# Kernel tuning notes

Measured on AMD Instinct MI355X. Metric: run time of the kernel, lower is better.

The kernel has to match this reference:

```python
import jax, jax.numpy as jnp
import numpy as np
import math

D_MODEL = 2048
NUM_HEADS = 16
D_HEAD = D_MODEL // NUM_HEADS
ROPE_BASE = 10000.0

def _rope(t, pos):
    # t: [b, h, T, d_head]; standard rotate-half RoPE with base 10000.
    T, d = t.shape[-2], t.shape[-1]
    start = max(pos, 0)  # pos < 0 means training / position 0
    inv_freq = 1.0 / (ROPE_BASE ** (jnp.arange(0, d, 2, dtype=jnp.float32) / d))  # [d/2]
    positions = jnp.arange(start, start + T, dtype=jnp.float32)                   # [T]
    ang = positions[:, None] * inv_freq[None, :]                                  # [T, d/2]
    cos, sin = jnp.cos(ang), jnp.sin(ang)
    x1, x2 = t[..., : d // 2], t[..., d // 2 :]
    return jnp.concatenate([x1 * cos - x2 * sin, x1 * sin + x2 * cos], axis=-1)

def setup_inputs() -> dict:
    key = jax.random.key(0)
    kx, kq, kk, kv, kw = jax.random.split(key, 5)
    s = 1.0 / math.sqrt(D_MODEL)
    return {
        "x": jax.random.normal(kx, (2, 2048, D_MODEL), dtype=jnp.float32),
        "q_out": jax.random.normal(kq, (D_MODEL, D_MODEL), dtype=jnp.float32) * s,
        "k_out": jax.random.normal(kk, (D_MODEL, D_MODEL), dtype=jnp.float32) * s,
        "v_out": jax.random.normal(kv, (D_MODEL, D_MODEL), dtype=jnp.float32) * s,
        "w_out": jax.random.normal(kw, (D_MODEL, D_MODEL), dtype=jnp.float32) * s,
        "pos": 0,
    }

def reference(x, q_out, k_out, v_out, w_out, pos):
    b, t, d = x.shape
    h, dh = NUM_HEADS, D_HEAD

    def heads(y):  # [b, t, d] -> [b, h, t, dh]
        return y.reshape(b, t, h, dh).transpose(0, 2, 1, 3)

    q = _rope(heads(jnp.einsum('btd,de->bte', x, q_out)), pos)
    k = _rope(heads(jnp.einsum('btd,de->bte', x, k_out)), pos)
    v = heads(jnp.einsum('btd,de->bte', x, v_out))

    score = jnp.einsum('bhqd,bhkd->bhqk', q, k) / math.sqrt(dh)
    causal = jnp.triu(jnp.ones((t, t), dtype=bool), k=1)  # True above diagonal -> masked
    score = jnp.where(causal, -jnp.inf, score)
    weights = jax.nn.softmax(score, axis=-1)
    ctx = jnp.einsum('bhqk,bhkd->bhqd', weights, v)        # [b, h, t, dh]
    ctx = ctx.transpose(0, 2, 1, 3).reshape(b, t, d)
    return jnp.einsum('btd,de->bte', ctx, w_out)
```

## Files before the change

kernel.cpp:

```cpp
#include <hip/hip_runtime.h>
#include <hip/hip_bf16.h>
#include <math.h>

#define NH 16
#define DH 128
#define DM 2048
#define BB 2
#define TT 2048

typedef unsigned short u16;
typedef __attribute__((ext_vector_type(8))) __bf16 bf16x8;
typedef __attribute__((ext_vector_type(8))) u16 u16x8;
typedef __attribute__((ext_vector_type(4))) u16 u16x4;
typedef __attribute__((ext_vector_type(4))) float f32x4;

__device__ __forceinline__ float bf2f(u16 a){
  union { unsigned u; float f; } v; v.u = ((unsigned)a) << 16; return v.f;
}
__device__ __forceinline__ u16 f2bf(float f){
  union { float f; unsigned u; } v; v.f = f;
  unsigned r = v.u + 0x7fffu + ((v.u >> 16) & 1u);
  return (u16)(r >> 16);
}
__device__ __forceinline__ __bf16 f2bfh(float f){
  u16 r = f2bf(f); __bf16 h; __builtin_memcpy(&h, &r, 2); return h;
}
__device__ __forceinline__ float bfh2f(__bf16 h){
  u16 r; __builtin_memcpy(&r, &h, 2); return bf2f(r);
}

typedef const __attribute__((address_space(1))) unsigned int* gas_p;
typedef __attribute__((address_space(3))) unsigned int* las_p;
__device__ __forceinline__ void gl_lds16(const u16* g, u16* lds_uniform_base){
  __builtin_amdgcn_global_load_lds((gas_p)(const void*)g,
                                   (las_p)(void*)lds_uniform_base, 16, 0, 0);
}

#define SB() do{ asm volatile("" ::: "memory"); \
                 __builtin_amdgcn_s_barrier();  \
                 asm volatile("" ::: "memory"); }while(0)
#define WAITV8 asm volatile("s_waitcnt vmcnt(8)" ::: "memory")
#define WAITV0 asm volatile("s_waitcnt vmcnt(0)" ::: "memory")

__global__ __launch_bounds__(256)
void prep4(const float* __restrict__ w0, const float* __restrict__ w1,
           const float* __restrict__ w2, const float* __restrict__ x,
           u16* __restrict__ dst, u16* __restrict__ xb){
  __shared__ u16 tile[32][33];
  const int z = blockIdx.z;
  const int tx = threadIdx.x, ty = threadIdx.y;
  if (z == 3){
    const int bid = blockIdx.y * 64 + blockIdx.x;
    const int tid = ty * 32 + tx;
    #pragma unroll
    for (int rep = 0; rep < 2; rep++){
      const int i = bid * 512 + rep * 256 + tid;
      const f32x4 v = *(const f32x4*)(x + (size_t)i * 4);
      u16x4 o;
      #pragma unroll
      for (int j = 0; j < 4; j++) o[j] = f2bf(v[j]);
      *(u16x4*)(xb + (size_t)i * 4) = o;
    }
    return;
  }
  const float* W = (z == 0) ? w0 : (z == 1) ? w1 : w2;
  u16* Wt = dst + (size_t)z * DM * DM;
  const int bx = blockIdx.x * 32, by = blockIdx.y * 32;
  #pragma unroll
  for (int i = 0; i < 32; i += 8)
    tile[ty + i][tx] = f2bf(W[(size_t)(by + ty + i) * DM + bx + tx]);
  __syncthreads();
  #pragma unroll
  for (int i = 0; i < 32; i += 8)
    Wt[(size_t)(bx + ty + i) * DM + by + tx] = tile[tx][ty + i];
}

__global__ __launch_bounds__(256)
void transpose2048(const float* __restrict__ W, u16* __restrict__ Wt){
  __shared__ u16 tile[32][33];
  const int tx = threadIdx.x, ty = threadIdx.y;
  const int bx = blockIdx.x * 32, by = blockIdx.y * 32;
  #pragma unroll
  for (int i = 0; i < 32; i += 8)
    tile[ty + i][tx] = f2bf(W[(size_t)(by + ty + i) * DM + bx + tx]);
  __syncthreads();
  #pragma unroll
  for (int i = 0; i < 32; i += 8)
    Wt[(size_t)(bx + ty + i) * DM + by + tx] = tile[tx][ty + i];
}

__global__ __launch_bounds__(256)
void cvt_f32_bf16(const float* __restrict__ src, u16* __restrict__ dst, int n4){
  const int i = blockIdx.x * 256 + threadIdx.x;
  if (i >= n4) return;
  const f32x4 v = *(const f32x4*)(src + (size_t)i * 4);
  u16x4 o;
  #pragma unroll
  for (int j = 0; j < 4; j++) o[j] = f2bf(v[j]);
  *(u16x4*)(dst + (size_t)i * 4) = o;
}

__global__ __launch_bounds__(256)
void gemm_bt(const u16* __restrict__ A, const u16* __restrict__ Bt_base,
             void* __restrict__ C0, u16* __restrict__ Ck, u16* __restrict__ Cv,
             int mode0){
  __shared__ u16 As[2][128][32];
  __shared__ u16 Bs[2][128][32];
  const int z = blockIdx.z;
  const u16* Bt = Bt_base + (size_t)z * DM * DM;
  void* C = (z == 0) ? C0 : (z == 1) ? (void*)Ck : (void*)Cv;
  const int mode = (z == 0) ? mode0 : (z == 1) ? 3 : 2;

  const int tid = threadIdx.x;
  const int wave = tid >> 6, lane = tid & 63;
  const int wm = wave & 1, wn = wave >> 1;
  const int row16 = lane & 15, quad = lane >> 4;
  const int m0 = blockIdx.x * 128, n0 = blockIdx.y * 128;

  const f32x4 zero = {0.f, 0.f, 0.f, 0.f};
  f32x4 acc[4][4];
  #pragma unroll
  for (int i = 0; i < 4; i++)
    #pragma unroll
    for (int j = 0; j < 4; j++) acc[i][j] = zero;

  const int srow = lane >> 2;
  const int scol = (lane & 3) * 8;

  for (int k0 = 0; k0 < DM; k0 += 64){
    #pragma unroll
    for (int c = 0; c < 2; c++){
      const int rbase = wave * 32 + c * 16;
      const u16* pa = A  + (size_t)(m0 + rbase + srow) * DM + k0 + scol;
      const u16* pb = Bt + (size_t)(n0 + rbase + srow) * DM + k0 + scol;
      gl_lds16(pa,      &As[0][rbase][0]);
      gl_lds16(pa + 32, &As[1][rbase][0]);
      gl_lds16(pb,      &Bs[0][rbase][0]);
      gl_lds16(pb + 32, &Bs[1][rbase][0]);
    }
    __syncthreads();
    #pragma unroll
    for (int buf = 0; buf < 2; buf++){
      bf16x8 af[4], bfr[4];
      #pragma unroll
      for (int mt = 0; mt < 4; mt++)
        af[mt] = *(const bf16x8*)&As[buf][wm * 64 + mt * 16 + row16][quad * 8];
      #pragma unroll
      for (int nt = 0; nt < 4; nt++)
        bfr[nt] = *(const bf16x8*)&Bs[buf][wn * 64 + nt * 16 + row16][quad * 8];
      #pragma unroll
      for (int mt = 0; mt < 4; mt++)
        #pragma unroll
        for (int nt = 0; nt < 4; nt++)
          acc[mt][nt] = __builtin_amdgcn_mfma_f32_16x16x32_bf16(af[mt], bfr[nt], acc[mt][nt], 0, 0, 0);
    }
    __syncthreads();
  }

  #pragma unroll
  for (int mt = 0; mt < 4; mt++){
    #pragma unroll
    for (int nt = 0; nt < 4; nt++){
      #pragma unroll
      for (int r = 0; r < 4; r++){
        const int m = m0 + wm * 64 + mt * 16 + quad * 4 + r;
        const int n = n0 + wn * 64 + nt * 16 + row16;
        const int b = m >> 11, t = m & (TT - 1);
        const int hh = n >> 7, dh = n & (DH - 1);
        if (mode == 1){
          ((u16*)C)[(((size_t)(b * NH + hh) * TT + t) * DH) + dh] = f2bf(acc[mt][nt][r]);
        } else if (mode == 3){
          const int dhs = dh ^ ((t & 7) << 3);
          ((u16*)C)[(((size_t)(b * NH + hh) * TT + t) * DH) + dhs] = f2bf(acc[mt][nt][r]);
        } else if (mode == 2){
          const int ts = (t & 63) ^ ((dh & 7) << 3);
          ((u16*)C)[(((size_t)(b * NH + hh) * 32 + (t >> 6)) * 8192) + dh * 64 + ts] = f2bf(acc[mt][nt][r]);
        } else {
          ((float*)C)[(size_t)m * DM + n] = acc[mt][nt][r];
        }
      }
    }
  }
}

__global__ __launch_bounds__(256)
void ropek(u16* __restrict__ kb, const int* __restrict__ posp){
  const int idx = blockIdx.x * 256 + threadIdx.x;
  const int pair = idx & 63;
  const int row = idx >> 6;
  const int t = row & (TT - 1);
  int p0 = *posp; if (p0 < 0) p0 = 0;
  const float tf = (float)(p0 + t);
  const size_t base = (size_t)row * DH;
  const int pl = pair ^ ((t & 7) << 3);
  const float inv = __expf(-(float)pl * (9.2103403719761836f / 64.f));
  const float a = tf * inv;
  const float sn = __sinf(a), cs = __cosf(a);
  const float k1 = bf2f(kb[base + pair]);
  const float k2 = bf2f(kb[base + 64 + pair]);
  kb[base + pair]      = f2bf(k1 * cs - k2 * sn);
  kb[base + 64 + pair] = f2bf(k1 * sn + k2 * cs);
}

template<bool MASK>
__device__ __forceinline__ void attn_tile(
    int kt0, int qbase, int wave, int row16, int quad,
    const bf16x8 (&qf)[4],
    u16 (&k_s)[64][128], u16 (&vt_s)[128][64], u16 (&p_s)[4][16][68],
    f32x4 (&o_acc)[8], float (&l_acc)[4])
{
  const float scale = 0.08838834764831845f;
  const f32x4 zero = {0.f, 0.f, 0.f, 0.f};
  const int fx = (row16 & 7) << 3;
  f32x4 s_acc[4];
  #pragma unroll
  for (int nt = 0; nt < 4; nt++) s_acc[nt] = zero;
  __builtin_amdgcn_s_setprio(1);
  #pragma unroll
  for (int st = 0; st < 4; st++)
    #pragma unroll
    for (int nt = 0; nt < 4; nt++){
      const bf16x8 kf = *(const bf16x8*)&k_s[nt * 16 + row16][(st * 32 + quad * 8) ^ fx];
      s_acc[nt] = __builtin_amdgcn_mfma_f32_16x16x32_bf16(qf[st], kf, s_acc[nt], 0, 0, 0);
    }
  __builtin_amdgcn_s_setprio(0);
  #pragma unroll
  for (int r = 0; r < 4; r++){
    float ps = 0.f;
    #pragma unroll
    for (int nt = 0; nt < 4; nt++){
      float p = __expf(s_acc[nt][r] * scale);
      if (MASK){
        const int qr = qbase + quad * 4 + r;
        if (kt0 + nt * 16 + row16 > qr) p = 0.f;
      }
      ps += p;
      p_s[wave][quad * 4 + r][nt * 16 + row16] = f2bf(p);
    }
    l_acc[r] += ps;
  }
  asm volatile("" ::: "memory");

  __builtin_amdgcn_s_setprio(1);
  #pragma unroll
  for (int kk = 0; kk < 2; kk++){
    const bf16x8 pf = *(const bf16x8*)&p_s[wave][row16][kk * 32 + quad * 8];
    #pragma unroll
    for (int nd = 0; nd < 8; nd++){
      const bf16x8 vb = *(const bf16x8*)&vt_s[nd * 16 + row16][(kk * 32 + quad * 8) ^ fx];
      o_acc[nd] = __builtin_amdgcn_mfma_f32_16x16x32_bf16(pf, vb, o_acc[nd], 0, 0, 0);
    }
  }
  __builtin_amdgcn_s_setprio(0);
}

__device__ __forceinline__ void attn_pass(
    const u16* __restrict__ q, const u16* __restrict__ k,
    const u16* __restrict__ vtg, u16* __restrict__ ctx,
    int q0, int bh, int p0, int wave, int lane, int row16, int quad,
    u16 (&k_s)[2][64][128], u16 (&vt_s)[2][128][64], u16 (&p_s)[4][16][68])
{
  const size_t bho = (size_t)bh * TT * DH;
  const int qbase = q0 + wave * 16;
  const int nt = (q0 >> 6) + 1;

  bf16x8 qf[4];
  {
    const u16* qp = q + bho + (size_t)(qbase + row16) * DH + quad * 8;
    #pragma unroll
    for (int st = 0; st < 4; st++) qf[st] = *(const bf16x8*)(qp + st * 32);
  }
  {
    const float tf = (float)(p0 + qbase + row16);
    #pragma unroll
    for (int st = 0; st < 2; st++){
      #pragma unroll
      for (int j = 0; j < 8; j++){
        const int dh = st * 32 + quad * 8 + j;
        const float inv = __expf(-(float)dh * (9.2103403719761836f / 64.f));
        const float a = tf * inv;
        const float sn = __sinf(a), cs = __cosf(a);
        const float lo = bfh2f(qf[st][j]), hi = bfh2f(qf[st + 2][j]);
        qf[st][j]     = f2bfh(lo * cs - hi * sn);
        qf[st + 2][j] = f2bfh(lo * sn + hi * cs);
      }
    }
  }

  float l_acc[4] = {0.f, 0.f, 0.f, 0.f};
  const f32x4 zero = {0.f, 0.f, 0.f, 0.f};
  f32x4 o_acc[8];
  #pragma unroll
  for (int i = 0; i < 8; i++) o_acc[i] = zero;

  const int kl_r = lane >> 4, kl_c = (lane & 15) * 8;
  const int vl_r = lane >> 3, vl_c = (lane & 7) * 8;

  #define ASTAGE(t, db) do{ \
    const int kt = (t) * 64; \
    _Pragma("unroll") \
    for (int i = 0; i < 4; i++){ \
      const int rb = wave * 16 + i * 4; \
      gl_lds16(k + bho + (size_t)(kt + rb + kl_r) * DH + kl_c, &k_s[db][rb][0]); \
    } \
    const u16* vpan = vtg + ((size_t)bh * 32 + (t)) * 8192; \
    _Pragma("unroll") \
    for (int i = 0; i < 4; i++){ \
      const int rb = wave * 32 + i * 8; \
      gl_lds16(vpan + (size_t)(rb + vl_r) * 64 + vl_c, &vt_s[db][rb][0]); \
    } \
  }while(0)

  ASTAGE(0, 0);
  for (int t = 0; t < nt; ++t){
    const int db = t & 1;
    if (t + 1 < nt){
      ASTAGE(t + 1, db ^ 1);
      WAITV8;
    } else {
      WAITV0;
    }
    SB();
    if (t < nt - 1)
      attn_tile<false>(t * 64, qbase, wave, row16, quad, qf, k_s[db], vt_s[db], p_s, o_acc, l_acc);
    else
      attn_tile<true >(t * 64, qbase, wave, row16, quad, qf, k_s[db], vt_s[db], p_s, o_acc, l_acc);
    SB();
  }
  #undef ASTAGE

  #pragma unroll
  for (int r = 0; r < 4; r++){
    #pragma unroll
    for (int off = 1; off < 16; off <<= 1) l_acc[r] += __shfl_xor(l_acc[r], off, 64);
  }

  const int b = bh >> 4, h = bh & 15;
  #pragma unroll
  for (int nd = 0; nd < 8; nd++){
    #pragma unroll
    for (int r = 0; r < 4; r++){
      const int qr = qbase + quad * 4 + r;
      const size_t off = ((size_t)b * TT + qr) * DM + h * DH + nd * 16 + row16;
      ctx[off] = f2bf(o_acc[nd][r] / l_acc[r]);
    }
  }
}

__global__ __launch_bounds__(256)
void attn_fwd(const u16* __restrict__ q, const u16* __restrict__ k,
              const u16* __restrict__ vtg, u16* __restrict__ ctx,
              const int* __restrict__ posp){
  __shared__ u16 k_s[2][64][128];
  __shared__ u16 vt_s[2][128][64];
  __shared__ u16 p_s[4][16][68];
  const int tid = threadIdx.x;
  const int wave = tid >> 6, lane = tid & 63;
  const int row16 = lane & 15, quad = lane >> 4;
  const int i = blockIdx.x;
  const int bh = blockIdx.y;
  int p0 = *posp; if (p0 < 0) p0 = 0;

  attn_pass(q, k, vtg, ctx, (31 - i) * 64, bh, p0, wave, lane, row16, quad, k_s, vt_s, p_s);
  attn_pass(q, k, vtg, ctx, i * 64,        bh, p0, wave, lane, row16, quad, k_s, vt_s, p_s);
}

extern "C" void kernel_launch(void* const* d_in, const int* in_sizes, int n_in,
                              void* d_out, int out_size, void* d_ws, size_t ws_size,
                              hipStream_t stream){
  const float* x  = (const float*)d_in[0];
  const float* wq = (const float*)d_in[1];
  const float* wk = (const float*)d_in[2];
  const float* wv = (const float*)d_in[3];
  const float* wo = (const float*)d_in[4];
  const int* pos  = (const int*)d_in[5];

  char* ws = (char*)d_ws;
  const dim3 tg(64, 64), tb(32, 8);

  if (ws_size >= 92274688ull){
    u16* xb  = (u16*)ws;                  u16* cb = xb;
    u16* wt3 = (u16*)(ws + 16777216);
    u16* qb  = (u16*)(ws + 41943040);
    u16* kb  = (u16*)(ws + 58720256);
    u16* vtg = (u16*)(ws + 75497472);

    prep4<<<dim3(64, 64, 4), tb, 0, stream>>>(wq, wk, wv, x, wt3, xb);
    gemm_bt<<<dim3(32, 16, 3), 256, 0, stream>>>(xb, wt3, qb, kb, vtg, 1);
    transpose2048<<<tg, tb, 0, stream>>>(wo, wt3);
    ropek<<<16384, 256, 0, stream>>>(kb, pos);
    attn_fwd<<<dim3(16, 32), 256, 0, stream>>>(qb, kb, vtg, cb, pos);
    gemm_bt<<<dim3(32, 16, 1), 256, 0, stream>>>(cb, wt3, d_out, 0, 0, 0);
  } else {
    u16* xb  = (u16*)ws;                  u16* cb = xb;
    u16* wt  = (u16*)(ws + 16777216);
    u16* qb  = (u16*)(ws + 25165824);
    u16* kb  = (u16*)(ws + 41943040);
    u16* vtg = (u16*)(ws + 58720256);

    cvt_f32_bf16<<<8192, 256, 0, stream>>>(x, xb, 2097152);
    transpose2048<<<tg, tb, 0, stream>>>(wq, wt);
    gemm_bt<<<dim3(32, 16, 1), 256, 0, stream>>>(xb, wt, qb, 0, 0, 1);
    transpose2048<<<tg, tb, 0, stream>>>(wk, wt);
    gemm_bt<<<dim3(32, 16, 1), 256, 0, stream>>>(xb, wt, kb, 0, 0, 3);
    transpose2048<<<tg, tb, 0, stream>>>(wv, wt);
    gemm_bt<<<dim3(32, 16, 1), 256, 0, stream>>>(xb, wt, vtg, 0, 0, 2);
    ropek<<<16384, 256, 0, stream>>>(kb, pos);
    attn_fwd<<<dim3(16, 32), 256, 0, stream>>>(qb, kb, vtg, cb, pos);
    transpose2048<<<tg, tb, 0, stream>>>(wo, wt);
    gemm_bt<<<dim3(32, 16, 1), 256, 0, stream>>>(cb, wt, d_out, 0, 0, 0);
  }
}
```

Before: 407.1 us.

## Merge paired causal attention passes to share K/V tile loads; vectorize K RoPE

Each attention block handles a high and a low query tile. The two sequential passes become one loop over key tiles, so every K/V tile staged into LDS serves both query tiles and the low tile's loads are no longer fetched twice. This roughly halves the K/V global traffic per block and the number of barrier iterations. The cost is two sets of Q fragments and output accumulators held in registers, which may lower occupancy or cause spills. Separately, the K RoPE kernel now handles 8 pairs per thread with 16-byte vector loads and stores, launching 8x fewer blocks.

```diff
diff --git a/kernel.cpp b/kernel.cpp
--- a/kernel.cpp
+++ b/kernel.cpp
@@ -186,20 +186,27 @@
 __global__ __launch_bounds__(256)
 void ropek(u16* __restrict__ kb, const int* __restrict__ posp){
   const int idx = blockIdx.x * 256 + threadIdx.x;
-  const int pair = idx & 63;
-  const int row = idx >> 6;
+  const int sub = idx & 7;
+  const int row = idx >> 3;
   const int t = row & (TT - 1);
   int p0 = *posp; if (p0 < 0) p0 = 0;
   const float tf = (float)(p0 + t);
-  const size_t base = (size_t)row * DH;
-  const int pl = pair ^ ((t & 7) << 3);
-  const float inv = __expf(-(float)pl * (9.2103403719761836f / 64.f));
-  const float a = tf * inv;
-  const float sn = __sinf(a), cs = __cosf(a);
-  const float k1 = bf2f(kb[base + pair]);
-  const float k2 = bf2f(kb[base + 64 + pair]);
-  kb[base + pair]      = f2bf(k1 * cs - k2 * sn);
-  kb[base + 64 + pair] = f2bf(k1 * sn + k2 * cs);
+  const size_t base = (size_t)row * DH + sub * 8;
+  u16x8 lo = *(const u16x8*)(kb + base);
+  u16x8 hi = *(const u16x8*)(kb + base + 64);
+  const int fx = (t & 7) << 3;
+  #pragma unroll
+  for (int j = 0; j < 8; j++){
+    const int pl = (sub * 8 + j) ^ fx;
+    const float inv = __expf(-(float)pl * (9.2103403719761836f / 64.f));
+    const float a = tf * inv;
+    const float sn = __sinf(a), cs = __cosf(a);
+    const float k1 = bf2f(lo[j]), k2 = bf2f(hi[j]);
+    lo[j] = f2bf(k1 * cs - k2 * sn);
+    hi[j] = f2bf(k1 * sn + k2 * cs);
+  }
+  *(u16x8*)(kb + base)      = lo;
+  *(u16x8*)(kb + base + 64) = hi;
 }
 
 template<bool MASK>
@@ -254,87 +261,38 @@
   __builtin_amdgcn_s_setprio(0);
 }
 
-__device__ __forceinline__ void attn_pass(
-    const u16* __restrict__ q, const u16* __restrict__ k,
-    const u16* __restrict__ vtg, u16* __restrict__ ctx,
-    int q0, int bh, int p0, int wave, int lane, int row16, int quad,
-    u16 (&k_s)[2][64][128], u16 (&vt_s)[2][128][64], u16 (&p_s)[4][16][68])
+__device__ __forceinline__ void qload_rope(
+    const u16* __restrict__ q, size_t bho, int qbase, int p0,
+    int row16, int quad, bf16x8 (&qf)[4])
 {
-  const size_t bho = (size_t)bh * TT * DH;
-  const int qbase = q0 + wave * 16;
-  const int nt = (q0 >> 6) + 1;
-
-  bf16x8 qf[4];
-  {
-    const u16* qp = q + bho + (size_t)(qbase + row16) * DH + quad * 8;
-    #pragma unroll
-    for (int st = 0; st < 4; st++) qf[st] = *(const bf16x8*)(qp + st * 32);
-  }
-  {
-    const float tf = (float)(p0 + qbase + row16);
-    #pragma unroll
-    for (int st = 0; st < 2; st++){
-      #pragma unroll
-      for (int j = 0; j < 8; j++){
-        const int dh = st * 32 + quad * 8 + j;
-        const float inv = __expf(-(float)dh * (9.2103403719761836f / 64.f));
-        const float a = tf * inv;
-        const float sn = __sinf(a), cs = __cosf(a);
-        const float lo = bfh2f(qf[st][j]), hi = bfh2f(qf[st + 2][j]);
-        qf[st][j]     = f2bfh(lo * cs - hi * sn);
-        qf[st + 2][j] = f2bfh(lo * sn + hi * cs);
-      }
-    }
-  }
-
-  float l_acc[4] = {0.f, 0.f, 0.f, 0.f};
-  const f32x4 zero = {0.f, 0.f, 0.f, 0.f};
-  f32x4 o_acc[8];
-  #pragma unroll
-  for (int i = 0; i < 8; i++) o_acc[i] = zero;
-
-  const int kl_r = lane >> 4, kl_c = (lane & 15) * 8;
-  const int vl_r = lane >> 3, vl_c = (lane & 7) * 8;
-
-  #define ASTAGE(t, db) do{ \
-    const int kt = (t) * 64; \
-    _Pragma("unroll") \
-    for (int i = 0; i < 4; i++){ \
-      const int rb = wave * 16 + i * 4; \
-      gl_lds16(k + bho + (size_t)(kt + rb + kl_r) * DH + kl_c, &k_s[db][rb][0]); \
-    } \
-    const u16* vpan = vtg + ((size_t)bh * 32 + (t)) * 8192; \
-    _Pragma("unroll") \
-    for (int i = 0; i < 4; i++){ \
-      const int rb = wave * 32 + i * 8; \
-      gl_lds16(vpan + (size_t)(rb + vl_r) * 64 + vl_c, &vt_s[db][rb][0]); \
-    } \
-  }while(0)
-
-  ASTAGE(0, 0);
-  for (int t = 0; t < nt; ++t){
-    const int db = t & 1;
-    if (t + 1 < nt){
-      ASTAGE(t + 1, db ^ 1);
-      WAITV8;
-    } else {
-      WAITV0;
-    }
-    SB();
-    if (t < nt - 1)
-      attn_tile<false>(t * 64, qbase, wave, row16, quad, qf, k_s[db], vt_s[db], p_s, o_acc, l_acc);
-    else
-      attn_tile<true >(t * 64, qbase, wave, row16, quad, qf, k_s[db], vt_s[db], p_s, o_acc, l_acc);
-    SB();
-  }
-  #undef ASTAGE
-
+  const u16* qp = q + bho + (size_t)(qbase + row16) * DH + quad * 8;
+  #pragma unroll
+  for (int st = 0; st < 4; st++) qf[st] = *(const bf16x8*)(qp + st * 32);
+  const float tf = (float)(p0 + qbase + row16);
+  #pragma unroll
+  for (int st = 0; st < 2; st++){
+    #pragma unroll
+    for (int j = 0; j < 8; j++){
+      const int dh = st * 32 + quad * 8 + j;
+      const float inv = __expf(-(float)dh * (9.2103403719761836f / 64.f));
+      const float a = tf * inv;
+      const float sn = __sinf(a), cs = __cosf(a);
+      const float lo = bfh2f(qf[st][j]), hi = bfh2f(qf[st + 2][j]);
+      qf[st][j]     = f2bfh(lo * cs - hi * sn);
+      qf[st + 2][j] = f2bfh(lo * sn + hi * cs);
+    }
+  }
+}
+
+__device__ __forceinline__ void owrite(
+    u16* __restrict__ ctx, int bh, int qbase, int row16, int quad,
+    f32x4 (&o_acc)[8], float (&l_acc)[4])
+{
   #pragma unroll
   for (int r = 0; r < 4; r++){
     #pragma unroll
     for (int off = 1; off < 16; off <<= 1) l_acc[r] += __shfl_xor(l_acc[r], off, 64);
   }
-
   const int b = bh >> 4, h = bh & 15;
   #pragma unroll
   for (int nd = 0; nd < 8; nd++){
@@ -360,9 +318,64 @@
   const int i = blockIdx.x;
   const int bh = blockIdx.y;
   int p0 = *posp; if (p0 < 0) p0 = 0;
-
-  attn_pass(q, k, vtg, ctx, (31 - i) * 64, bh, p0, wave, lane, row16, quad, k_s, vt_s, p_s);
-  attn_pass(q, k, vtg, ctx, i * 64,        bh, p0, wave, lane, row16, quad, k_s, vt_s, p_s);
+  const size_t bho = (size_t)bh * TT * DH;
+
+  const int qbH = (31 - i) * 64 + wave * 16;
+  const int qbL = i * 64 + wave * 16;
+  const int nT = 32 - i;
+
+  bf16x8 qfH[4], qfL[4];
+  qload_rope(q, bho, qbH, p0, row16, quad, qfH);
+  qload_rope(q, bho, qbL, p0, row16, quad, qfL);
+
+  float lH[4] = {0.f, 0.f, 0.f, 0.f}, lL[4] = {0.f, 0.f, 0.f, 0.f};
+  const f32x4 zero = {0.f, 0.f, 0.f, 0.f};
+  f32x4 oH[8], oL[8];
+  #pragma unroll
+  for (int j = 0; j < 8; j++){ oH[j] = zero; oL[j] = zero; }
+
+  const int kl_r = lane >> 4, kl_c = (lane & 15) * 8;
+  const int vl_r = lane >> 3, vl_c = (lane & 7) * 8;
+
+  #define ASTAGE(t, db) do{ \
+    const int kt = (t) * 64; \
+    _Pragma("unroll") \
+    for (int u = 0; u < 4; u++){ \
+      const int rb = wave * 16 + u * 4; \
+      gl_lds16(k + bho + (size_t)(kt + rb + kl_r) * DH + kl_c, &k_s[db][rb][0]); \
+    } \
+    const u16* vpan = vtg + ((size_t)bh * 32 + (t)) * 8192; \
+    _Pragma("unroll") \
+    for (int u = 0; u < 4; u++){ \
+      const int rb = wave * 32 + u * 8; \
+      gl_lds16(vpan + (size_t)(rb + vl_r) * 64 + vl_c, &vt_s[db][rb][0]); \
+    } \
+  }while(0)
+
+  ASTAGE(0, 0);
+  for (int t = 0; t < nT; ++t){
+    const int db = t & 1;
+    if (t + 1 < nT){
+      ASTAGE(t + 1, db ^ 1);
+      WAITV8;
+    } else {
+      WAITV0;
+    }
+    SB();
+    if (t < nT - 1)
+      attn_tile<false>(t * 64, qbH, wave, row16, quad, qfH, k_s[db], vt_s[db], p_s, oH, lH);
+    else
+      attn_tile<true >(t * 64, qbH, wave, row16, quad, qfH, k_s[db], vt_s[db], p_s, oH, lH);
+    if (t < i)
+      attn_tile<false>(t * 64, qbL, wave, row16, quad, qfL, k_s[db], vt_s[db], p_s, oL, lL);
+    else if (t == i)
+      attn_tile<true >(t * 64, qbL, wave, row16, quad, qfL, k_s[db], vt_s[db], p_s, oL, lL);
+    SB();
+  }
+  #undef ASTAGE
+
+  owrite(ctx, bh, qbH, row16, quad, oH, lH);
+  owrite(ctx, bh, qbL, row16, quad, oL, lL);
 }
 
 extern "C" void kernel_launch(void* const* d_in, const int* in_sizes, int n_in,
@@ -388,7 +401,7 @@
     prep4<<<dim3(64, 64, 4), tb, 0, stream>>>(wq, wk, wv, x, wt3, xb);
     gemm_bt<<<dim3(32, 16, 3), 256, 0, stream>>>(xb, wt3, qb, kb, vtg, 1);
     transpose2048<<<tg, tb, 0, stream>>>(wo, wt3);
-    ropek<<<16384, 256, 0, stream>>>(kb, pos);
+    ropek<<<2048, 256, 0, stream>>>(kb, pos);
     attn_fwd<<<dim3(16, 32), 256, 0, stream>>>(qb, kb, vtg, cb, pos);
     gemm_bt<<<dim3(32, 16, 1), 256, 0, stream>>>(cb, wt3, d_out, 0, 0, 0);
   } else {
@@ -405,7 +418,7 @@
     gemm_bt<<<dim3(32, 16, 1), 256, 0, stream>>>(xb, wt, kb, 0, 0, 3);
     transpose2048<<<tg, tb, 0, stream>>>(wv, wt);
     gemm_bt<<<dim3(32, 16, 1), 256, 0, stream>>>(xb, wt, vtg, 0, 0, 2);
-    ropek<<<16384, 256, 0, stream>>>(kb, pos);
+    ropek<<<2048, 256, 0, stream>>>(kb, pos);
     attn_fwd<<<dim3(16, 32), 256, 0, stream>>>(qb, kb, vtg, cb, pos);
     transpose2048<<<tg, tb, 0, stream>>>(wo, wt);
     gemm_bt<<<dim3(32, 16, 1), 256, 0, stream>>>(cb, wt, d_out, 0, 0, 0);
```

Result: no change. 405.7 us (-0.3%).
